# Kernel tuning notes

Measured on AMD Instinct MI355X. Metric: run time of the kernel, lower is better.

## Reference

```python
import jax, jax.numpy as jnp
import numpy as np

WS = 8      # window size
SHIFT = 4   # cyclic shift = WS // 2
NH = 4      # num heads
DIM = 128
RES = 32    # cubic volume side
N = WS ** 3 # tokens per window


def _win_part_np(x, ws):
    B, D, H, W, C = x.shape
    x = x.reshape(B, D // ws, ws, H // ws, ws, W // ws, ws, C)
    return x.transpose(0, 1, 3, 5, 2, 4, 6, 7).reshape(-1, ws ** 3, C)


def _make_mask(d, h, w, ws, ss):
    # Swin-style shifted-window attention mask (compute_mask in source)
    img = np.zeros((1, d, h, w, 1), np.float32)
    cnt = 0
    sls = (slice(0, -ws), slice(-ws, -ss), slice(-ss, None))
    for a in sls:
        for b in sls:
            for c in sls:
                img[:, a, b, c, :] = cnt
                cnt += 1
    mw = _win_part_np(img, ws)[..., 0]          # (nW, N)
    diff = mw[:, None, :] - mw[:, :, None]      # (nW, N, N)
    return np.where(diff != 0, -100.0, 0.0).astype(np.float32)


def _rel_index(ws):
    coords = np.stack(np.meshgrid(np.arange(ws), np.arange(ws), np.arange(ws), indexing='ij')).reshape(3, -1)
    rel = (coords[:, :, None] - coords[:, None, :]).transpose(1, 2, 0) + (ws - 1)
    L = 2 * ws - 1
    return (rel[..., 0] * L * L + rel[..., 1] * L + rel[..., 2]).astype(np.int32)  # (N, N)


def _coords_table(ws):
    # SwinV2 continuous log-spaced relative coordinates table
    r = np.arange(-(ws - 1), ws, dtype=np.float32)
    t = np.stack(np.meshgrid(r, r, r, indexing='ij'), axis=-1) / (ws - 1) * 8.0
    return np.sign(t) * np.log2(np.abs(t) + 1.0) / np.log2(8.0)  # (2w-1, 2w-1, 2w-1, 3)


MASK = jnp.asarray(_make_mask(RES, RES, RES, WS, SHIFT))      # (nW_per_batch, N, N)
REL_IDX = jnp.asarray(_rel_index(WS))                          # (N, N)
CTAB = jnp.asarray(_coords_table(WS).reshape(-1, 3))           # ((2w-1)^3, 3)


def _ln(x, w, b, eps=1e-5):
    mu = x.mean(-1, keepdims=True)
    var = ((x - mu) ** 2).mean(-1, keepdims=True)
    return (x - mu) * jax.lax.rsqrt(var + eps) * w + b


def _win_part(x, ws):
    B, D, H, W, C = x.shape
    x = x.reshape(B, D // ws, ws, H // ws, ws, W // ws, ws, C)
    return x.transpose(0, 1, 3, 5, 2, 4, 6, 7).reshape(-1, ws ** 3, C)


def _win_rev(w, ws, B, D, H, Wd):
    C = w.shape[-1]
    x = w.reshape(B, D // ws, H // ws, Wd // ws, ws, ws, ws, C)
    return x.transpose(0, 1, 4, 2, 5, 3, 6, 7).reshape(B, D, H, Wd, C)


def _forward(x, norm1_w, norm1_b, qkv_w, qkv_b, logit_scale, cpb_w1, cpb_b1, cpb_w2,
             proj_w, proj_b, norm2_w, norm2_b, fc1_w, fc1_b, fc2_w, fc2_b):
    B, D, H, Wd, C = x.shape
    hd = C // NH
    nWpb = (D // WS) * (H // WS) * (Wd // WS)
    # cyclic shift + window partition
    shifted = jnp.roll(x, (-SHIFT, -SHIFT, -SHIFT), axis=(1, 2, 3))
    xw = _win_part(shifted, WS)                                  # (nW, N, C)
    qkv = (xw @ qkv_w.T + qkv_b).reshape(-1, N, 3, NH, hd).transpose(2, 0, 3, 1, 4)
    q, k, v = qkv[0], qkv[1], qkv[2]                             # (nW, NH, N, hd)
    # SwinV2 cosine attention with learned temperature
    qn = q / (jnp.linalg.norm(q, axis=-1, keepdims=True) + 1e-12)
    kn = k / (jnp.linalg.norm(k, axis=-1, keepdims=True) + 1e-12)
    scale = jnp.exp(jnp.minimum(logit_scale, jnp.log(100.0)))
    attn = jnp.einsum('whnd,whmd->whnm', qn, kn) * scale
    # continuous relative position bias via small MLP over log-spaced coords
    bt = jax.nn.relu(CTAB @ cpb_w1.T + cpb_b1) @ cpb_w2.T        # ((2w-1)^3, NH)
    bias = 16.0 * jax.nn.sigmoid(bt[REL_IDX])                    # (N, N, NH)
    attn = attn + bias.transpose(2, 0, 1)[None]
    # shifted-window mask
    attn = attn.reshape(B, nWpb, NH, N, N) + MASK[None, :, None]
    attn = jax.nn.softmax(attn, axis=-1).reshape(-1, NH, N, N)
    out = jnp.einsum('whnm,whmd->whnd', attn, v).transpose(0, 2, 1, 3).reshape(-1, N, C)
    out = out @ proj_w.T + proj_b
    out = _win_rev(out, WS, B, D, H, Wd)
    out = jnp.roll(out, (SHIFT, SHIFT, SHIFT), axis=(1, 2, 3))
    # SwinV2 post-norm residuals
    x = x + _ln(out, norm1_w, norm1_b)
    h = jax.nn.gelu(x @ fc1_w.T + fc1_b)
    m = h @ fc2_w.T + fc2_b
    return x + _ln(m, norm2_w, norm2_b)


def setup_inputs():
    key = jax.random.key(0)
    ks = jax.random.split(key, 8)
    g = lambda k, s: jax.random.normal(k, s, jnp.float32) * 0.02
    return {
        'x': jax.random.normal(ks[0], (1, RES, RES, RES, DIM), jnp.float32),
        'norm1_w': jnp.ones((DIM,), jnp.float32), 'norm1_b': jnp.zeros((DIM,), jnp.float32),
        'qkv_w': g(ks[1], (3 * DIM, DIM)), 'qkv_b': jnp.zeros((3 * DIM,), jnp.float32),
        'logit_scale': jnp.log(10.0) * jnp.ones((NH, 1, 1), jnp.float32),
        'cpb_w1': g(ks[2], (512, 3)), 'cpb_b1': jnp.zeros((512,), jnp.float32),
        'cpb_w2': g(ks[3], (NH, 512)),
        'proj_w': g(ks[4], (DIM, DIM)), 'proj_b': jnp.zeros((DIM,), jnp.float32),
        'norm2_w': jnp.ones((DIM,), jnp.float32), 'norm2_b': jnp.zeros((DIM,), jnp.float32),
        'fc1_w': g(ks[5], (4 * DIM, DIM)), 'fc1_b': jnp.zeros((4 * DIM,), jnp.float32),
        'fc2_w': g(ks[6], (DIM, 4 * DIM)), 'fc2_b': jnp.zeros((DIM,), jnp.float32),
    }


def reference(x, norm1_w, norm1_b, qkv_w, qkv_b, logit_scale, cpb_w1, cpb_b1, cpb_w2,
              proj_w, proj_b, norm2_w, norm2_b, fc1_w, fc1_b, fc2_w, fc2_b):
    return _forward(x, norm1_w, norm1_b, qkv_w, qkv_b, logit_scale, cpb_w1, cpb_b1, cpb_w2,
                    proj_w, proj_b, norm2_w, norm2_b, fc1_w, fc1_b, fc2_w, fc2_b)
```

## Files before the change

kernel.cpp:

```cpp
#include <hip/hip_runtime.h>
#include <hip/hip_fp16.h>
#include <math.h>


typedef short bf16x8 __attribute__((ext_vector_type(8)));
typedef float f32x4 __attribute__((ext_vector_type(4)));

__device__ __forceinline__ int regionOf(int wb, int a) {
    return (wb < 3) ? 0 : ((a < 4) ? 1 : 2);
}

__device__ __forceinline__ unsigned short f2bf(float f) {
    unsigned int u = __float_as_uint(f);
    u += 0x7fffu + ((u >> 16) & 1u);
    return (unsigned short)(u >> 16);
}

__global__ void k_bias_table(const float* __restrict__ w1, const float* __restrict__ b1,
                             const float* __restrict__ w2, float* __restrict__ BT) {
    int e = blockIdx.x;
    int id = e / 225, rem = e % 225, ih = rem / 15, iw = rem % 15;
    float ct[3];
    int ids[3] = {id, ih, iw};
#pragma unroll
    for (int a = 0; a < 3; ++a) {
        float r = (float)(ids[a] - 7) * (8.0f / 7.0f);
        float s = (r > 0.f) ? 1.f : ((r < 0.f) ? -1.f : 0.f);
        ct[a] = s * log2f(fabsf(r) + 1.0f) * (1.0f / 3.0f);
    }
    int t = threadIdx.x;
    float acc[4] = {0.f, 0.f, 0.f, 0.f};
    for (int j = t; j < 512; j += 128) {
        float hv = ct[0] * w1[j * 3 + 0] + ct[1] * w1[j * 3 + 1] + ct[2] * w1[j * 3 + 2] + b1[j];
        hv = fmaxf(hv, 0.f);
#pragma unroll
        for (int h = 0; h < 4; ++h) acc[h] += hv * w2[h * 512 + j];
    }
    __shared__ float red[4][128];
#pragma unroll
    for (int h = 0; h < 4; ++h) red[h][t] = acc[h];
    __syncthreads();
    if (t < 4) {
        float s = 0.f;
        for (int i = 0; i < 128; ++i) s += red[t][i];
        BT[e * 4 + t] = 16.0f / (1.0f + expf(-s));
    }
}

__global__ void k_bias_expand(const float* __restrict__ BT, __half* __restrict__ B4T) {
    int idx = blockIdx.x * 256 + threadIdx.x;
    int n = idx >> 9, m = idx & 511;
    int an = n >> 6, bn = (n >> 3) & 7, cn = n & 7;
    int am = m >> 6, bm = (m >> 3) & 7, cm = m & 7;
    int ridx = ((an - am + 7) * 15 + (bn - bm + 7)) * 15 + (cn - cm + 7);
    float4 bv = *(const float4*)(BT + ridx * 4);
    B4T[(size_t)(0 * 512 + n) * 512 + m] = __float2half(bv.x);
    B4T[(size_t)(1 * 512 + n) * 512 + m] = __float2half(bv.y);
    B4T[(size_t)(2 * 512 + n) * 512 + m] = __float2half(bv.z);
    B4T[(size_t)(3 * 512 + n) * 512 + m] = __float2half(bv.w);
}

__global__ void k_maskbits(unsigned long long* __restrict__ MQ) {
    int idx = blockIdx.x * 256 + threadIdx.x;
    int word = idx & 7, n = (idx >> 3) & 511, w = idx >> 12;
    int wd = w >> 4, wh = (w >> 2) & 3, ww = w & 3;
    int a = n >> 6, b = (n >> 3) & 7, c = n & 7;
    int cq = regionOf(wd, a) * 9 + regionOf(wh, b) * 3 + regionOf(ww, c);
    unsigned long long bits = 0ull;
    for (int j = 0; j < 64; ++j) {
        int m = word * 64 + j;
        int am = m >> 6, bm = (m >> 3) & 7, cm = m & 7;
        int cmv = regionOf(wd, am) * 9 + regionOf(wh, bm) * 3 + regionOf(ww, cm);
        if (cmv == cq) bits |= (1ull << j);
    }
    MQ[idx] = bits;
}

__device__ __forceinline__ void packw(const float* __restrict__ src, unsigned short* __restrict__ dst,
                                      int o, int K, int KK) {
    int lane_ = (o >> 3) & 63, e = o & 7, tl = o >> 9;
    int kk = tl % KK, t = tl / KK;
    int oc = t * 16 + (lane_ & 15);
    int k = kk * 32 + 8 * (lane_ >> 4) + e;
    dst[o] = f2bf(src[(size_t)oc * K + k]);
}

__global__ void k_wcvt(const float* __restrict__ w1, const float* __restrict__ w2,
                       const float* __restrict__ qw, const float* __restrict__ pw,
                       unsigned short* __restrict__ W1f, unsigned short* __restrict__ W2f,
                       unsigned short* __restrict__ Wqf, unsigned short* __restrict__ Pwf) {
    int idx = blockIdx.x * 256 + threadIdx.x;
    packw(w1, W1f, idx, 128, 4);
    packw(w2, W2f, idx, 512, 16);
    if (idx < 49152) packw(qw, Wqf, idx, 128, 4);
    if (idx < 16384) packw(pw, Pwf, idx, 128, 4);
}

__global__ void __launch_bounds__(256) k_qkv(
    const float* __restrict__ x, const unsigned short* __restrict__ Wqf,
    const float* __restrict__ qb, const float* __restrict__ ls,
    unsigned short* __restrict__ Qb, unsigned short* __restrict__ Kb,
    unsigned short* __restrict__ Vt) {
    const int tid = threadIdx.x;
    const int wv = tid >> 6, lane = tid & 63;
    const int qL = lane & 15, g = lane >> 4;
    const int tokG = blockIdx.x * 64 + wv * 16;
    const int w = tokG >> 9, n0 = tokG & 511;
    const int wd = w >> 4, wh = (w >> 2) & 3, ww = w & 3;
    const int n = n0 + qL;
    const int a = n >> 6, b = (n >> 3) & 7, c = n & 7;
    const int od = (wd * 8 + a + 4) & 31, oh = (wh * 8 + b + 4) & 31, ow = (ww * 8 + c + 4) & 31;
    const float* xrow = x + ((od * 32 + oh) * 32 + ow) * 128;

    bf16x8 bX[4];
#pragma unroll
    for (int kk = 0; kk < 4; ++kk) {
        float4 f0 = *(const float4*)(xrow + kk * 32 + 8 * g);
        float4 f1 = *(const float4*)(xrow + kk * 32 + 8 * g + 4);
        bf16x8 v;
        v[0] = (short)f2bf(f0.x); v[1] = (short)f2bf(f0.y);
        v[2] = (short)f2bf(f0.z); v[3] = (short)f2bf(f0.w);
        v[4] = (short)f2bf(f1.x); v[5] = (short)f2bf(f1.y);
        v[6] = (short)f2bf(f1.z); v[7] = (short)f2bf(f1.w);
        bX[kk] = v;
    }

#pragma unroll
    for (int s = 0; s < 2; ++s) {
        unsigned short* dst = s ? Kb : Qb;
#pragma unroll
        for (int ci = 0; ci < 4; ++ci) {
            const int ch0 = s * 128 + ci * 32;
            const int tileL = ch0 >> 4;
            f32x4 aL = {0.f, 0.f, 0.f, 0.f}, aH = {0.f, 0.f, 0.f, 0.f};
#pragma unroll
            for (int kk = 0; kk < 4; ++kk) {
                bf16x8 wL = *(const bf16x8*)(Wqf + (size_t)(tileL * 4 + kk) * 512 + lane * 8);
                bf16x8 wH = *(const bf16x8*)(Wqf + (size_t)((tileL + 1) * 4 + kk) * 512 + lane * 8);
                aL = __builtin_amdgcn_mfma_f32_16x16x32_bf16(wL, bX[kk], aL, 0, 0, 0);
                aH = __builtin_amdgcn_mfma_f32_16x16x32_bf16(wH, bX[kk], aH, 0, 0, 0);
            }
            float4 bL = *(const float4*)(qb + ch0 + 4 * g);
            float4 bH = *(const float4*)(qb + ch0 + 16 + 4 * g);
            float vL[4], vH[4], ss = 0.f;
#pragma unroll
            for (int r = 0; r < 4; ++r) {
                vL[r] = aL[r] + ((const float*)&bL)[r];
                vH[r] = aH[r] + ((const float*)&bH)[r];
                ss += vL[r] * vL[r] + vH[r] * vH[r];
            }
            ss += __shfl_xor(ss, 16);
            ss += __shfl_xor(ss, 32);
            float rn = 1.0f / (sqrtf(ss) + 1e-12f);
            if (s == 0) rn *= expf(fminf(ls[ci], 4.6051701859880914f));
            unsigned int l0 = (unsigned int)f2bf(vL[0] * rn) | ((unsigned int)f2bf(vL[1] * rn) << 16);
            unsigned int l1 = (unsigned int)f2bf(vL[2] * rn) | ((unsigned int)f2bf(vL[3] * rn) << 16);
            unsigned int h0 = (unsigned int)f2bf(vH[0] * rn) | ((unsigned int)f2bf(vH[1] * rn) << 16);
            unsigned int h1 = (unsigned int)f2bf(vH[2] * rn) | ((unsigned int)f2bf(vH[3] * rn) << 16);
            size_t base = ((size_t)(w * 4 + ci) * 512 + n) * 32;
            *(uint2*)(dst + base + 4 * g) = make_uint2(l0, l1);
            *(uint2*)(dst + base + 16 + 4 * g) = make_uint2(h0, h1);
        }
    }
#pragma unroll
    for (int ci = 0; ci < 4; ++ci) {
        const int ch0 = 256 + ci * 32;
        const int tileL = ch0 >> 4;
        f32x4 aL = {0.f, 0.f, 0.f, 0.f}, aH = {0.f, 0.f, 0.f, 0.f};
#pragma unroll
        for (int kk = 0; kk < 4; ++kk) {
            bf16x8 wL = *(const bf16x8*)(Wqf + (size_t)(tileL * 4 + kk) * 512 + lane * 8);
            bf16x8 wH = *(const bf16x8*)(Wqf + (size_t)((tileL + 1) * 4 + kk) * 512 + lane * 8);
            aL = __builtin_amdgcn_mfma_f32_16x16x32_bf16(wL, bX[kk], aL, 0, 0, 0);
            aH = __builtin_amdgcn_mfma_f32_16x16x32_bf16(wH, bX[kk], aH, 0, 0, 0);
        }
        float4 bL = *(const float4*)(qb + ch0 + 4 * g);
        float4 bH = *(const float4*)(qb + ch0 + 16 + 4 * g);
        const size_t vtb = (size_t)(w * 4 + ci) * 32 * 512;
        const size_t nblk = (size_t)(n >> 3) * 256 + (n & 7);
#pragma unroll
        for (int r = 0; r < 4; ++r) {
            Vt[vtb + nblk + (size_t)(4 * g + r) * 8] = f2bf(aL[r] + ((const float*)&bL)[r]);
            Vt[vtb + nblk + (size_t)(16 + 4 * g + r) * 8] = f2bf(aH[r] + ((const float*)&bH)[r]);
        }
    }
}

__global__ void __launch_bounds__(256) k_attn(
    const unsigned short* __restrict__ Qb, const unsigned short* __restrict__ Kb,
    const unsigned short* __restrict__ Vt, const __half* __restrict__ B4T,
    const unsigned long long* __restrict__ MQ, unsigned short* __restrict__ AOb) {
    const int bid = blockIdx.x;
    const int cxd = bid & 7;
    const int r9 = bid >> 3;
    const int qoct = r9 & 7;
    const int gidx = (r9 >> 3) * 8 + cxd;
    const int h = gidx & 3;
    const int w = gidx >> 2;
    const int tid = threadIdx.x;
    const int wv = tid >> 6;
    const int lane = tid & 63;
    const int qL = lane & 15;
    const int g = lane >> 4;

    __shared__ __align__(16) unsigned short Pbuf[4][16][136];
    __shared__ __align__(16) __half Bstage[4][16][136];

    const int q0 = qoct * 64 + wv * 16;
    const int wh4 = w * 4 + h;
    const size_t qk_base = (size_t)wh4 * 512 * 32;
    const size_t vt_base = (size_t)wh4 * 32 * 512;

    bf16x8 bQ = *(const bf16x8*)(Qb + qk_base + (size_t)(q0 + qL) * 32 + 8 * g);

    const __half* Bw = B4T + ((size_t)h * 512 + q0) * 512;
    const unsigned long long* MQr = MQ + (size_t)(w * 512 + q0 + qL) * 8;
    unsigned short* prow = &Pbuf[wv][qL][0];
    const __half* brow = &Bstage[wv][qL][0];

    float m_run = -1e30f, l_run = 0.f;
    f32x4 o0 = {0.f, 0.f, 0.f, 0.f}, o1 = {0.f, 0.f, 0.f, 0.f};

    for (int c = 0; c < 4; ++c) {
        const int m0 = c * 128;
        float4 br[4];
#pragma unroll
        for (int i = 0; i < 4; ++i) {
            int f = i * 64 + lane;
            br[i] = *(const float4*)(Bw + (size_t)(f >> 4) * 512 + m0 + (f & 15) * 8);
        }
        uint4 mw = *(const uint4*)(MQr + 2 * c);
        unsigned long long mq0 = ((unsigned long long)mw.y << 32) | mw.x;
        unsigned long long mq1 = ((unsigned long long)mw.w << 32) | mw.z;

        f32x4 st[8];
#pragma unroll
        for (int t = 0; t < 8; ++t) {
            bf16x8 aK = *(const bf16x8*)(Kb + qk_base + (size_t)(m0 + t * 16 + qL) * 32 + 8 * g);
            st[t] = __builtin_amdgcn_mfma_f32_16x16x32_bf16(
                aK, bQ, (f32x4){0.f, 0.f, 0.f, 0.f}, 0, 0, 0);
        }
#pragma unroll
        for (int i = 0; i < 4; ++i) {
            int f = i * 64 + lane;
            *(float4*)&Bstage[wv][f >> 4][(f & 15) * 8] = br[i];
        }
        float cmax = -1e30f;
#pragma unroll
        for (int t = 0; t < 8; ++t) {
            float2 braw = *(const float2*)(brow + t * 16 + 4 * g);
            __half2 h01 = *reinterpret_cast<const __half2*>(&braw.x);
            __half2 h23 = *reinterpret_cast<const __half2*>(&braw.y);
            float2 b01 = __half22float2(h01);
            float2 b23 = __half22float2(h23);
            float bvv[4] = {b01.x, b01.y, b23.x, b23.y};
            unsigned long long word = (t < 4) ? mq0 : mq1;
            int bshift = (t & 3) * 16 + 4 * g;
#pragma unroll
            for (int r = 0; r < 4; ++r) {
                float sv = st[t][r] + bvv[r];
                if (!((word >> (bshift + r)) & 1ull)) sv -= 100.f;
                st[t][r] = sv;
                cmax = fmaxf(cmax, sv);
            }
        }
        cmax = fmaxf(cmax, __shfl_xor(cmax, 16));
        cmax = fmaxf(cmax, __shfl_xor(cmax, 32));
        float mnew = fmaxf(m_run, cmax);
        float corr = __expf(m_run - mnew);
        float csum = 0.f;
#pragma unroll
        for (int t = 0; t < 8; ++t) {
#pragma unroll
            for (int r = 0; r < 4; ++r) {
                float p = __expf(st[t][r] - mnew);
                st[t][r] = p;
                csum += p;
            }
        }
        csum += __shfl_xor(csum, 16);
        csum += __shfl_xor(csum, 32);
        l_run = l_run * corr + csum;
        m_run = mnew;
#pragma unroll
        for (int r = 0; r < 4; ++r) {
            float cr = __shfl(corr, 4 * g + r, 64);
            o0[r] *= cr;
            o1[r] *= cr;
        }
#pragma unroll
        for (int t = 0; t < 8; ++t) {
            unsigned int lo = (unsigned int)f2bf(st[t][0]) | ((unsigned int)f2bf(st[t][1]) << 16);
            unsigned int hi = (unsigned int)f2bf(st[t][2]) | ((unsigned int)f2bf(st[t][3]) << 16);
            *(uint2*)(prow + t * 16 + 4 * g) = make_uint2(lo, hi);
        }
#pragma unroll
        for (int s = 0; s < 4; ++s) {
            const size_t vblk = vt_base + (size_t)(((m0 + s * 32) >> 3) + g) * 256;
            bf16x8 pa = *(const bf16x8*)(prow + s * 32 + 8 * g);
            bf16x8 bv0 = *(const bf16x8*)(Vt + vblk + (size_t)qL * 8);
            bf16x8 bv1 = *(const bf16x8*)(Vt + vblk + (size_t)(16 + qL) * 8);
            o0 = __builtin_amdgcn_mfma_f32_16x16x32_bf16(pa, bv0, o0, 0, 0, 0);
            o1 = __builtin_amdgcn_mfma_f32_16x16x32_bf16(pa, bv1, o1, 0, 0, 0);
        }
    }
    float linv = 1.0f / l_run;
#pragma unroll
    for (int r = 0; r < 4; ++r) {
        float lr = __shfl(linv, 4 * g + r, 64);
        int q = q0 + 4 * g + r;
        AOb[(size_t)(w * 512 + q) * 128 + h * 32 + qL] = f2bf(o0[r] * lr);
        AOb[(size_t)(w * 512 + q) * 128 + h * 32 + 16 + qL] = f2bf(o1[r] * lr);
    }
}

__global__ void __launch_bounds__(256) k_proj_ln(
    const unsigned short* __restrict__ AOb, const unsigned short* __restrict__ Pwf,
    const float* __restrict__ pb, const float* __restrict__ n1w, const float* __restrict__ n1b,
    const float* __restrict__ x, float* __restrict__ out, unsigned short* __restrict__ Xb) {
    const int tid = threadIdx.x;
    const int wv = tid >> 6, lane = tid & 63;
    const int qL = lane & 15, g = lane >> 4;
    const int tokG = blockIdx.x * 64 + wv * 16;
    const int tok = tokG + qL;
    const int w = tokG >> 9;
    const int n = (tokG & 511) + qL;
    const int wd = w >> 4, wh = (w >> 2) & 3, ww = w & 3;

    bf16x8 bA[4];
#pragma unroll
    for (int kk = 0; kk < 4; ++kk)
        bA[kk] = *(const bf16x8*)(AOb + (size_t)tok * 128 + kk * 32 + 8 * g);

    f32x4 acc[8];
#pragma unroll
    for (int t = 0; t < 8; ++t) acc[t] = (f32x4){0.f, 0.f, 0.f, 0.f};
#pragma unroll
    for (int t = 0; t < 8; ++t) {
#pragma unroll
        for (int kk = 0; kk < 4; ++kk) {
            bf16x8 wf = *(const bf16x8*)(Pwf + (size_t)(t * 4 + kk) * 512 + lane * 8);
            acc[t] = __builtin_amdgcn_mfma_f32_16x16x32_bf16(wf, bA[kk], acc[t], 0, 0, 0);
        }
    }

    float y[8][4];
    float s = 0.f, ssq = 0.f;
#pragma unroll
    for (int t = 0; t < 8; ++t) {
        float4 pbv = *(const float4*)(pb + t * 16 + 4 * g);
#pragma unroll
        for (int r = 0; r < 4; ++r) {
            float v = acc[t][r] + ((const float*)&pbv)[r];
            y[t][r] = v;
            s += v;
            ssq += v * v;
        }
    }
    s += __shfl_xor(s, 16);
    s += __shfl_xor(s, 32);
    ssq += __shfl_xor(ssq, 16);
    ssq += __shfl_xor(ssq, 32);
    float mean = s * (1.0f / 128.0f);
    float var = ssq * (1.0f / 128.0f) - mean * mean;
    float rstd = rsqrtf(var + 1e-5f);

    int a = n >> 6, b = (n >> 3) & 7, c = n & 7;
    int od = (wd * 8 + a + 4) & 31, oh = (wh * 8 + b + 4) & 31, ow = (ww * 8 + c + 4) & 31;
    int off = ((od * 32 + oh) * 32 + ow) * 128;
#pragma unroll
    for (int t = 0; t < 8; ++t) {
        int col = t * 16 + 4 * g;
        float4 wn = *(const float4*)(n1w + col);
        float4 bn = *(const float4*)(n1b + col);
        float4 xr = *(const float4*)(x + off + col);
        float4 o;
        o.x = xr.x + (y[t][0] - mean) * rstd * wn.x + bn.x;
        o.y = xr.y + (y[t][1] - mean) * rstd * wn.y + bn.y;
        o.z = xr.z + (y[t][2] - mean) * rstd * wn.z + bn.z;
        o.w = xr.w + (y[t][3] - mean) * rstd * wn.w + bn.w;
        *(float4*)(out + off + col) = o;
        unsigned int p0 = (unsigned int)f2bf(o.x) | ((unsigned int)f2bf(o.y) << 16);
        unsigned int p1 = (unsigned int)f2bf(o.z) | ((unsigned int)f2bf(o.w) << 16);
        *(uint2*)(Xb + off + col) = make_uint2(p0, p1);
    }
}

__global__ void __launch_bounds__(256) k_fc1(
    const unsigned short* __restrict__ Xb, const unsigned short* __restrict__ W1f,
    const float* __restrict__ b1f, unsigned short* __restrict__ Hb) {
    const int tid = threadIdx.x;
    const int wv = tid >> 6, lane = tid & 63;
    const int qL = lane & 15, g = lane >> 4;
    const int tok = blockIdx.x * 64 + wv * 16 + qL;
    const int ocbase = blockIdx.y * 256;

    bf16x8 bX[4];
#pragma unroll
    for (int kk = 0; kk < 4; ++kk)
        bX[kk] = *(const bf16x8*)(Xb + (size_t)tok * 128 + kk * 32 + 8 * g);

#pragma unroll
    for (int t = 0; t < 16; ++t) {
        const int oc0 = ocbase + t * 16;
        const int tile = (ocbase >> 4) + t;
        f32x4 a1 = {0.f, 0.f, 0.f, 0.f};
#pragma unroll
        for (int kk = 0; kk < 4; ++kk) {
            bf16x8 w1v = *(const bf16x8*)(W1f + (size_t)(tile * 4 + kk) * 512 + lane * 8);
            a1 = __builtin_amdgcn_mfma_f32_16x16x32_bf16(w1v, bX[kk], a1, 0, 0, 0);
        }
        float4 b1v = *(const float4*)(b1f + oc0 + 4 * g);
        unsigned short hb[4];
#pragma unroll
        for (int r = 0; r < 4; ++r) {
            float v = a1[r] + ((const float*)&b1v)[r];
            float u = 0.7978845608028654f * (v + 0.044715f * v * v * v);
            u = fminf(u, 15.0f);
            float e = __expf(2.0f * u);
            hb[r] = f2bf(v * e / (e + 1.0f));
        }
        unsigned int lo = (unsigned int)hb[0] | ((unsigned int)hb[1] << 16);
        unsigned int hi = (unsigned int)hb[2] | ((unsigned int)hb[3] << 16);
        *(uint2*)(Hb + (size_t)tok * 512 + oc0 + 4 * g) = make_uint2(lo, hi);
    }
}

__global__ void __launch_bounds__(256) k_fc2(
    const unsigned short* __restrict__ Hb, const unsigned short* __restrict__ W2f,
    const float* __restrict__ b2f, const float* __restrict__ n2w,
    const float* __restrict__ n2b, float* __restrict__ out) {
    const int tid = threadIdx.x;
    const int wv = tid >> 6, lane = tid & 63;
    const int qL = lane & 15, g = lane >> 4;
    const int tg = wv >> 1;
    const int kh = wv & 1;
    const int tok = blockIdx.x * 32 + tg * 16 + qL;

    __shared__ __align__(16) float P[2][16][132];

    bf16x8 bH[8];
#pragma unroll
    for (int kk = 0; kk < 8; ++kk)
        bH[kk] = *(const bf16x8*)(Hb + (size_t)tok * 512 + kh * 256 + kk * 32 + 8 * g);

    f32x4 accM[8];
#pragma unroll
    for (int t = 0; t < 8; ++t) accM[t] = (f32x4){0.f, 0.f, 0.f, 0.f};
#pragma unroll
    for (int t2 = 0; t2 < 8; ++t2) {
#pragma unroll
        for (int kk = 0; kk < 8; ++kk) {
            bf16x8 w2v = *(const bf16x8*)(W2f + (size_t)(t2 * 16 + kh * 8 + kk) * 512 + lane * 8);
            accM[t2] = __builtin_amdgcn_mfma_f32_16x16x32_bf16(w2v, bH[kk], accM[t2], 0, 0, 0);
        }
    }

    if (kh == 1) {
#pragma unroll
        for (int t2 = 0; t2 < 8; ++t2)
            *(float4*)&P[tg][qL][t2 * 16 + 4 * g] = *(float4*)&accM[t2];
    }
    __syncthreads();
    if (kh == 0) {
        float y[8][4];
        float s = 0.f, ssq = 0.f;
#pragma unroll
        for (int t2 = 0; t2 < 8; ++t2) {
            float4 pv = *(const float4*)&P[tg][qL][t2 * 16 + 4 * g];
            float4 b2v = *(const float4*)(b2f + t2 * 16 + 4 * g);
#pragma unroll
            for (int r = 0; r < 4; ++r) {
                float v = accM[t2][r] + ((const float*)&pv)[r] + ((const float*)&b2v)[r];
                y[t2][r] = v;
                s += v;
                ssq += v * v;
            }
        }
        s += __shfl_xor(s, 16);
        s += __shfl_xor(s, 32);
        ssq += __shfl_xor(ssq, 16);
        ssq += __shfl_xor(ssq, 32);
        float mean = s * (1.0f / 128.0f);
        float var = ssq * (1.0f / 128.0f) - mean * mean;
        float rstd = rsqrtf(var + 1e-5f);
#pragma unroll
        for (int t2 = 0; t2 < 8; ++t2) {
            const int oc = t2 * 16 + 4 * g;
            float4 wn = *(const float4*)(n2w + oc);
            float4 bn = *(const float4*)(n2b + oc);
            float4 xr = *(const float4*)(out + (size_t)tok * 128 + oc);
            float4 o;
            o.x = xr.x + (y[t2][0] - mean) * rstd * wn.x + bn.x;
            o.y = xr.y + (y[t2][1] - mean) * rstd * wn.y + bn.y;
            o.z = xr.z + (y[t2][2] - mean) * rstd * wn.z + bn.z;
            o.w = xr.w + (y[t2][3] - mean) * rstd * wn.w + bn.w;
            *(float4*)(out + (size_t)tok * 128 + oc) = o;
        }
    }
}

extern "C" void kernel_launch(void* const* d_in, const int* in_sizes, int n_in, void* d_out,
                              int out_size, void* d_ws, size_t ws_size, hipStream_t stream) {
    const float* x   = (const float*)d_in[0];
    const float* n1w = (const float*)d_in[1];
    const float* n1b = (const float*)d_in[2];
    const float* qw  = (const float*)d_in[3];
    const float* qb  = (const float*)d_in[4];
    const float* ls  = (const float*)d_in[5];
    const float* cw1 = (const float*)d_in[6];
    const float* cb1 = (const float*)d_in[7];
    const float* cw2 = (const float*)d_in[8];
    const float* pw  = (const float*)d_in[9];
    const float* pb  = (const float*)d_in[10];
    const float* n2w = (const float*)d_in[11];
    const float* n2b = (const float*)d_in[12];
    const float* w1  = (const float*)d_in[13];
    const float* b1f = (const float*)d_in[14];
    const float* w2  = (const float*)d_in[15];
    const float* b2f = (const float*)d_in[16];
    float* out = (float*)d_out;

    float* ws = (float*)d_ws;
    float* BT = ws;
    __half* B4T = (__half*)(ws + 13504);
    unsigned long long* MQ = (unsigned long long*)(ws + 537792);
    unsigned short* Qb  = (unsigned short*)(ws + 1070272);
    unsigned short* Kb  = (unsigned short*)(ws + 3167424);
    unsigned short* Vt  = (unsigned short*)(ws + 5264576);
    unsigned short* AOb = (unsigned short*)(ws + 7361728);
    unsigned short* W1f = (unsigned short*)(ws + 9458880);
    unsigned short* W2f = (unsigned short*)(ws + 9491648);
    unsigned short* Wqf = (unsigned short*)(ws + 9524416);
    unsigned short* Pwf = (unsigned short*)(ws + 9548992);
    unsigned short* Xb  = (unsigned short*)(ws + 9557184);
    unsigned short* Hb  = (unsigned short*)(ws + 1070272);

    k_bias_table<<<3375, 128, 0, stream>>>(cw1, cb1, cw2, BT);
    k_bias_expand<<<1024, 256, 0, stream>>>(BT, B4T);
    k_maskbits<<<1024, 256, 0, stream>>>(MQ);
    k_wcvt<<<256, 256, 0, stream>>>(w1, w2, qw, pw, W1f, W2f, Wqf, Pwf);
    k_qkv<<<512, 256, 0, stream>>>(x, Wqf, qb, ls, Qb, Kb, Vt);
    k_attn<<<2048, 256, 0, stream>>>(Qb, Kb, Vt, B4T, MQ, AOb);
    k_proj_ln<<<512, 256, 0, stream>>>(AOb, Pwf, pb, n1w, n1b, x, out, Xb);
    k_fc1<<<dim3(512, 2), 256, 0, stream>>>(Xb, W1f, b1f, Hb);
    k_fc2<<<1024, 256, 0, stream>>>(Hb, W2f, b2f, n2w, n2b, out);
}
```

Baseline: 149.1 us.

## Split attention key range across wave pairs and merge softmax partials in LDS

Each attention block now covers 32 queries instead of 64, and two waves share each 16-query tile, each handling half of the 512 keys. Partial max, sum and output accumulators from the second half go through shared memory and are combined with a flash-style rescale before the write-out. The grid doubles to 4096 blocks, which shortens each wave's serial loop and adds parallelism. The cost is a block-wide sync, extra LDS traffic and duplicated Q loads.

```diff
diff --git a/kernel.cpp b/kernel.cpp
--- a/kernel.cpp
+++ b/kernel.cpp
@@ -193,20 +193,24 @@
     const int bid = blockIdx.x;
     const int cxd = bid & 7;
     const int r9 = bid >> 3;
-    const int qoct = r9 & 7;
-    const int gidx = (r9 >> 3) * 8 + cxd;
+    const int qhex = r9 & 15;
+    const int gidx = (r9 >> 4) * 8 + cxd;
     const int h = gidx & 3;
     const int w = gidx >> 2;
     const int tid = threadIdx.x;
     const int wv = tid >> 6;
+    const int qhalf = wv & 1;
+    const int mhalf = wv >> 1;
     const int lane = tid & 63;
     const int qL = lane & 15;
     const int g = lane >> 4;
 
     __shared__ __align__(16) unsigned short Pbuf[4][16][136];
     __shared__ __align__(16) __half Bstage[4][16][136];
-
-    const int q0 = qoct * 64 + wv * 16;
+    __shared__ float MB[2][16][2];
+    __shared__ float OB[2][16][36];
+
+    const int q0 = qhex * 32 + qhalf * 16;
     const int wh4 = w * 4 + h;
     const size_t qk_base = (size_t)wh4 * 512 * 32;
     const size_t vt_base = (size_t)wh4 * 32 * 512;
@@ -221,15 +225,15 @@
     float m_run = -1e30f, l_run = 0.f;
     f32x4 o0 = {0.f, 0.f, 0.f, 0.f}, o1 = {0.f, 0.f, 0.f, 0.f};
 
-    for (int c = 0; c < 4; ++c) {
-        const int m0 = c * 128;
+    for (int c = 0; c < 2; ++c) {
+        const int m0 = mhalf * 256 + c * 128;
         float4 br[4];
 #pragma unroll
         for (int i = 0; i < 4; ++i) {
             int f = i * 64 + lane;
             br[i] = *(const float4*)(Bw + (size_t)(f >> 4) * 512 + m0 + (f & 15) * 8);
         }
-        uint4 mw = *(const uint4*)(MQr + 2 * c);
+        uint4 mw = *(const uint4*)(MQr + 2 * (m0 >> 7));
         unsigned long long mq0 = ((unsigned long long)mw.y << 32) | mw.x;
         unsigned long long mq1 = ((unsigned long long)mw.w << 32) | mw.z;
 
@@ -304,13 +308,37 @@
             o1 = __builtin_amdgcn_mfma_f32_16x16x32_bf16(pa, bv1, o1, 0, 0, 0);
         }
     }
-    float linv = 1.0f / l_run;
-#pragma unroll
-    for (int r = 0; r < 4; ++r) {
-        float lr = __shfl(linv, 4 * g + r, 64);
-        int q = q0 + 4 * g + r;
-        AOb[(size_t)(w * 512 + q) * 128 + h * 32 + qL] = f2bf(o0[r] * lr);
-        AOb[(size_t)(w * 512 + q) * 128 + h * 32 + 16 + qL] = f2bf(o1[r] * lr);
+    if (mhalf == 1) {
+        if (g == 0) {
+            MB[qhalf][qL][0] = m_run;
+            MB[qhalf][qL][1] = l_run;
+        }
+#pragma unroll
+        for (int r = 0; r < 4; ++r) {
+            OB[qhalf][4 * g + r][qL] = o0[r];
+            OB[qhalf][4 * g + r][16 + qL] = o1[r];
+        }
+    }
+    __syncthreads();
+    if (mhalf == 0) {
+        float mB = MB[qhalf][qL][0];
+        float lB = MB[qhalf][qL][1];
+        float mN = fmaxf(m_run, mB);
+        float sA = __expf(m_run - mN);
+        float sB = __expf(mB - mN);
+        float linv = 1.0f / (l_run * sA + lB * sB);
+#pragma unroll
+        for (int r = 0; r < 4; ++r) {
+            int row = 4 * g + r;
+            float sAr = __shfl(sA, row, 64);
+            float sBr = __shfl(sB, row, 64);
+            float lr = __shfl(linv, row, 64);
+            int q = q0 + row;
+            float v0 = (o0[r] * sAr + OB[qhalf][row][qL] * sBr) * lr;
+            float v1 = (o1[r] * sAr + OB[qhalf][row][16 + qL] * sBr) * lr;
+            AOb[(size_t)(w * 512 + q) * 128 + h * 32 + qL] = f2bf(v0);
+            AOb[(size_t)(w * 512 + q) * 128 + h * 32 + 16 + qL] = f2bf(v1);
+        }
     }
 }
 
@@ -541,7 +569,7 @@
     k_maskbits<<<1024, 256, 0, stream>>>(MQ);
     k_wcvt<<<256, 256, 0, stream>>>(w1, w2, qw, pw, W1f, W2f, Wqf, Pwf);
     k_qkv<<<512, 256, 0, stream>>>(x, Wqf, qb, ls, Qb, Kb, Vt);
-    k_attn<<<2048, 256, 0, stream>>>(Qb, Kb, Vt, B4T, MQ, AOb);
+    k_attn<<<4096, 256, 0, stream>>>(Qb, Kb, Vt, B4T, MQ, AOb);
     k_proj_ln<<<512, 256, 0, stream>>>(AOb, Pwf, pb, n1w, n1b, x, out, Xb);
     k_fc1<<<dim3(512, 2), 256, 0, stream>>>(Xb, W1f, b1f, Hb);
     k_fc2<<<1024, 256, 0, stream>>>(Hb, W2f, b2f, n2w, n2b, out);
```

New measurement: 162.2 us. +8.8%, slower.

## Fold shift mask into per-window-type fp16 bias tables and drop mask bitfield

Applied to the files above, without the earlier changes.

The relative-position bias and the shifted-window mask are merged into 8 precombined fp16 tables, one per window boundary type (3 bits for the d/h/w edge). The separate mask-bit kernel and the per-element bit test in the attention softmax are removed. The attention kernel now picks its bias table from the window index. In exchange the expand kernel writes 8x more bias data (16 MB instead of 2 MB), and attention reads bias from 8 different tables, so it may cache less well.

```diff
diff --git a/kernel.cpp b/kernel.cpp
--- a/kernel.cpp
+++ b/kernel.cpp
@@ -47,33 +47,25 @@
     }
 }
 
-__global__ void k_bias_expand(const float* __restrict__ BT, __half* __restrict__ B4T) {
+__global__ void k_bias_expand(const float* __restrict__ BT, __half* __restrict__ B4M) {
     int idx = blockIdx.x * 256 + threadIdx.x;
-    int n = idx >> 9, m = idx & 511;
+    int m = idx & 511, n = (idx >> 9) & 511, ty = idx >> 18;
     int an = n >> 6, bn = (n >> 3) & 7, cn = n & 7;
     int am = m >> 6, bm = (m >> 3) & 7, cm = m & 7;
     int ridx = ((an - am + 7) * 15 + (bn - bm + 7)) * 15 + (cn - cm + 7);
     float4 bv = *(const float4*)(BT + ridx * 4);
-    B4T[(size_t)(0 * 512 + n) * 512 + m] = __float2half(bv.x);
-    B4T[(size_t)(1 * 512 + n) * 512 + m] = __float2half(bv.y);
-    B4T[(size_t)(2 * 512 + n) * 512 + m] = __float2half(bv.z);
-    B4T[(size_t)(3 * 512 + n) * 512 + m] = __float2half(bv.w);
-}
-
-__global__ void k_maskbits(unsigned long long* __restrict__ MQ) {
-    int idx = blockIdx.x * 256 + threadIdx.x;
-    int word = idx & 7, n = (idx >> 3) & 511, w = idx >> 12;
-    int wd = w >> 4, wh = (w >> 2) & 3, ww = w & 3;
-    int a = n >> 6, b = (n >> 3) & 7, c = n & 7;
-    int cq = regionOf(wd, a) * 9 + regionOf(wh, b) * 3 + regionOf(ww, c);
-    unsigned long long bits = 0ull;
-    for (int j = 0; j < 64; ++j) {
-        int m = word * 64 + j;
-        int am = m >> 6, bm = (m >> 3) & 7, cm = m & 7;
-        int cmv = regionOf(wd, am) * 9 + regionOf(wh, bm) * 3 + regionOf(ww, cm);
-        if (cmv == cq) bits |= (1ull << j);
-    }
-    MQ[idx] = bits;
+    int cq = ((ty & 4) ? ((an < 4) ? 1 : 2) : 0) * 9 +
+             ((ty & 2) ? ((bn < 4) ? 1 : 2) : 0) * 3 +
+             ((ty & 1) ? ((cn < 4) ? 1 : 2) : 0);
+    int cm_ = ((ty & 4) ? ((am < 4) ? 1 : 2) : 0) * 9 +
+              ((ty & 2) ? ((bm < 4) ? 1 : 2) : 0) * 3 +
+              ((ty & 1) ? ((cm < 4) ? 1 : 2) : 0);
+    float mk = (cq == cm_) ? 0.f : -100.f;
+    size_t nm = (size_t)n * 512 + m;
+    B4M[((size_t)(ty * 4 + 0) << 18) + nm] = __float2half(bv.x + mk);
+    B4M[((size_t)(ty * 4 + 1) << 18) + nm] = __float2half(bv.y + mk);
+    B4M[((size_t)(ty * 4 + 2) << 18) + nm] = __float2half(bv.z + mk);
+    B4M[((size_t)(ty * 4 + 3) << 18) + nm] = __float2half(bv.w + mk);
 }
 
 __device__ __forceinline__ void packw(const float* __restrict__ src, unsigned short* __restrict__ dst,
@@ -188,8 +180,8 @@
 
 __global__ void __launch_bounds__(256) k_attn(
     const unsigned short* __restrict__ Qb, const unsigned short* __restrict__ Kb,
-    const unsigned short* __restrict__ Vt, const __half* __restrict__ B4T,
-    const unsigned long long* __restrict__ MQ, unsigned short* __restrict__ AOb) {
+    const unsigned short* __restrict__ Vt, const __half* __restrict__ B4M,
+    unsigned short* __restrict__ AOb) {
     const int bid = blockIdx.x;
     const int cxd = bid & 7;
     const int r9 = bid >> 3;
@@ -213,8 +205,8 @@
 
     bf16x8 bQ = *(const bf16x8*)(Qb + qk_base + (size_t)(q0 + qL) * 32 + 8 * g);
 
-    const __half* Bw = B4T + ((size_t)h * 512 + q0) * 512;
-    const unsigned long long* MQr = MQ + (size_t)(w * 512 + q0 + qL) * 8;
+    const int ty = (((w >> 4) == 3) ? 4 : 0) | ((((w >> 2) & 3) == 3) ? 2 : 0) | (((w & 3) == 3) ? 1 : 0);
+    const __half* Bw = B4M + (((size_t)(ty * 4 + h) << 18)) + (size_t)q0 * 512;
     unsigned short* prow = &Pbuf[wv][qL][0];
     const __half* brow = &Bstage[wv][qL][0];
 
@@ -229,9 +221,6 @@
             int f = i * 64 + lane;
             br[i] = *(const float4*)(Bw + (size_t)(f >> 4) * 512 + m0 + (f & 15) * 8);
         }
-        uint4 mw = *(const uint4*)(MQr + 2 * c);
-        unsigned long long mq0 = ((unsigned long long)mw.y << 32) | mw.x;
-        unsigned long long mq1 = ((unsigned long long)mw.w << 32) | mw.z;
 
         f32x4 st[8];
 #pragma unroll
@@ -254,12 +243,9 @@
             float2 b01 = __half22float2(h01);
             float2 b23 = __half22float2(h23);
             float bvv[4] = {b01.x, b01.y, b23.x, b23.y};
-            unsigned long long word = (t < 4) ? mq0 : mq1;
-            int bshift = (t & 3) * 16 + 4 * g;
 #pragma unroll
             for (int r = 0; r < 4; ++r) {
                 float sv = st[t][r] + bvv[r];
-                if (!((word >> (bshift + r)) & 1ull)) sv -= 100.f;
                 st[t][r] = sv;
                 cmax = fmaxf(cmax, sv);
             }
@@ -523,25 +509,23 @@
 
     float* ws = (float*)d_ws;
     float* BT = ws;
-    __half* B4T = (__half*)(ws + 13504);
-    unsigned long long* MQ = (unsigned long long*)(ws + 537792);
-    unsigned short* Qb  = (unsigned short*)(ws + 1070272);
-    unsigned short* Kb  = (unsigned short*)(ws + 3167424);
-    unsigned short* Vt  = (unsigned short*)(ws + 5264576);
-    unsigned short* AOb = (unsigned short*)(ws + 7361728);
-    unsigned short* W1f = (unsigned short*)(ws + 9458880);
-    unsigned short* W2f = (unsigned short*)(ws + 9491648);
-    unsigned short* Wqf = (unsigned short*)(ws + 9524416);
-    unsigned short* Pwf = (unsigned short*)(ws + 9548992);
-    unsigned short* Xb  = (unsigned short*)(ws + 9557184);
-    unsigned short* Hb  = (unsigned short*)(ws + 1070272);
+    __half* B4M = (__half*)(ws + 13504);
+    unsigned short* Qb  = (unsigned short*)(ws + 4207808);
+    unsigned short* Kb  = (unsigned short*)(ws + 6304960);
+    unsigned short* Vt  = (unsigned short*)(ws + 8402112);
+    unsigned short* AOb = (unsigned short*)(ws + 10499264);
+    unsigned short* W1f = (unsigned short*)(ws + 12596416);
+    unsigned short* W2f = (unsigned short*)(ws + 12629184);
+    unsigned short* Wqf = (unsigned short*)(ws + 12661952);
+    unsigned short* Pwf = (unsigned short*)(ws + 12686528);
+    unsigned short* Xb  = (unsigned short*)(ws + 12694720);
+    unsigned short* Hb  = (unsigned short*)(ws + 4207808);
 
     k_bias_table<<<3375, 128, 0, stream>>>(cw1, cb1, cw2, BT);
-    k_bias_expand<<<1024, 256, 0, stream>>>(BT, B4T);
-    k_maskbits<<<1024, 256, 0, stream>>>(MQ);
+    k_bias_expand<<<8192, 256, 0, stream>>>(BT, B4M);
     k_wcvt<<<256, 256, 0, stream>>>(w1, w2, qw, pw, W1f, W2f, Wqf, Pwf);
     k_qkv<<<512, 256, 0, stream>>>(x, Wqf, qb, ls, Qb, Kb, Vt);
-    k_attn<<<2048, 256, 0, stream>>>(Qb, Kb, Vt, B4T, MQ, AOb);
+    k_attn<<<2048, 256, 0, stream>>>(Qb, Kb, Vt, B4M, AOb);
     k_proj_ln<<<512, 256, 0, stream>>>(AOb, Pwf, pb, n1w, n1b, x, out, Xb);
     k_fc1<<<dim3(512, 2), 256, 0, stream>>>(Xb, W1f, b1f, Hb);
     k_fc2<<<1024, 256, 0, stream>>>(Hb, W2f, b2f, n2w, n2b, out);
```

New measurement: 147.5 us. Within noise of the previous version (-1.1%).
